# Optimization experiments

Measured on AMD Instinct MI355X. Metric: run time of the kernel, lower is better.

Reference implementation:

```python
import jax, jax.numpy as jnp
import numpy as np

B, U = 64, 512          # batch, max_units
CORE, UNIT = 512, 256   # core_output_size, unit_embedding_size
HID, ACT = 1024, 12     # hidden_layer_size, ACTION_COUNT


def setup_inputs() -> dict:
    key = jax.random.key(0)
    ks = jax.random.split(key, 6)
    core_output = jax.random.normal(ks[0], (B, 1, CORE), dtype=jnp.float32)
    own_unit_embeddings = jax.random.normal(ks[1], (B, U, UNIT), dtype=jnp.float32)
    nr_units = jax.random.randint(ks[2], (B, 1), 0, U, dtype=jnp.int32)
    nr_own_flags = jax.random.randint(ks[3], (B, 1), 0, 64, dtype=jnp.int32)
    W1 = jax.random.normal(ks[4], (CORE + UNIT, HID), dtype=jnp.float32) * (1.0 / np.sqrt(CORE + UNIT))
    b1 = jnp.zeros((HID,), dtype=jnp.float32)
    W2 = jax.random.normal(ks[5], (HID, ACT), dtype=jnp.float32) * (1.0 / np.sqrt(HID))
    b2 = jnp.zeros((ACT,), dtype=jnp.float32)
    return {"core_output": core_output, "own_unit_embeddings": own_unit_embeddings,
            "nr_units": nr_units, "nr_own_flags": nr_own_flags,
            "W1": W1, "b1": b1, "W2": W2, "b2": b2}


def reference(core_output, own_unit_embeddings, nr_units, nr_own_flags, W1, b1, W2, b2):
    b, u, _ = own_unit_embeddings.shape
    # broadcast core output to every unit slot and concat along features: [B, U, UNIT+CORE]
    core_rep = jnp.broadcast_to(core_output, (b, u, core_output.shape[-1]))
    combined = jnp.concatenate([own_unit_embeddings, core_rep], axis=-1)
    autoregressive_embedding = jax.nn.relu(jnp.einsum('buf,fh->buh', combined, W1) + b1)
    logits = jnp.einsum('buh,ha->bua', autoregressive_embedding, W2) + b2
    action_probs = jax.nn.softmax(logits, axis=-1)
    # vectorized range mask: mask[i, f:n, :] = 1 else 1e-9
    idx = jnp.arange(u, dtype=nr_units.dtype)[None, :]        # [1, U]
    valid = (idx >= nr_own_flags) & (idx < nr_units)          # [B, U]
    mask = jnp.where(valid, 1.0, 1e-9).astype(action_probs.dtype)[:, :, None]
    return action_probs * mask, autoregressive_embedding
```

## Files before the change

kernel.cpp:

```cpp
#include <hip/hip_runtime.h>
#include <hip/hip_fp16.h>
#include <cstdint>

typedef unsigned short ushort_t;
typedef _Float16 f16x8 __attribute__((ext_vector_type(8)));
typedef float f32x4 __attribute__((ext_vector_type(4)));
typedef unsigned int u32x4 __attribute__((ext_vector_type(4)));

#define M_TOT  32768
#define K_EMB  256
#define K_CORE 512
#define ACT    12

__device__ __forceinline__ unsigned int pack2h(float a, float b) {
    __half2 h = __floats2half2_rn(a, b);
    union { __half2 h2; unsigned int u; } v; v.h2 = h; return v.u;
}

__global__ __launch_bounds__(1024) void prep_k(const float* __restrict__ W1,
                                               ushort_t* __restrict__ W1T,
                                               const float* __restrict__ core,
                                               const float* __restrict__ b1,
                                               float* __restrict__ cp) {
    __shared__ float tile[64][65];
    __shared__ float part[3][256];
    const int id = blockIdx.x;
    const int t = threadIdx.x;
    if (id < 64) {
        const int k0 = (id & 3) * 64, n0 = (id >> 2) * 64;
        const int r = t >> 4, c4 = (t & 15) * 4;
        const float4 v = *(const float4*)(W1 + (size_t)(k0 + r) * 1024 + n0 + c4);
        tile[r][c4 + 0] = v.x; tile[r][c4 + 1] = v.y;
        tile[r][c4 + 2] = v.z; tile[r][c4 + 3] = v.w;
        __syncthreads();
        uint2 o;
        o.x = pack2h(tile[c4 + 0][r], tile[c4 + 1][r]);
        o.y = pack2h(tile[c4 + 2][r], tile[c4 + 3][r]);
        *(uint2*)(W1T + (size_t)(n0 + r) * 256 + k0 + c4) = o;
    } else {
        const int xb = id - 64;
        const int b = xb >> 2;
        const int nl = t & 255;
        const int n = (xb & 3) * 256 + nl;
        const int kq = t >> 8;
        const float* cr = core + (size_t)b * K_CORE + kq * 128;
        const float* wp = W1 + (size_t)(K_EMB + kq * 128) * 1024 + n;
        float s0 = 0.f, s1 = 0.f, s2 = 0.f, s3 = 0.f;
#pragma unroll 8
        for (int k = 0; k < 128; k += 4) {
            s0 += cr[k + 0] * wp[(size_t)(k + 0) * 1024];
            s1 += cr[k + 1] * wp[(size_t)(k + 1) * 1024];
            s2 += cr[k + 2] * wp[(size_t)(k + 2) * 1024];
            s3 += cr[k + 3] * wp[(size_t)(k + 3) * 1024];
        }
        const float s = (s0 + s1) + (s2 + s3);
        if (kq) part[kq - 1][nl] = s;
        __syncthreads();
        if (kq == 0)
            cp[b * 1024 + n] = b1[n] + s + part[0][nl] + part[1][nl] + part[2][nl];
    }
}

__global__ __launch_bounds__(256, 3) void fused_k(const float* __restrict__ emb,
                                                  const ushort_t* __restrict__ w1t,
                                                  const float* __restrict__ cp,
                                                  const float* __restrict__ W2,
                                                  const float* __restrict__ b2,
                                                  const int* __restrict__ nr_units,
                                                  const int* __restrict__ nr_flags,
                                                  float* __restrict__ out0,
                                                  float* __restrict__ out1) {
    __shared__ __align__(16) ushort_t Asl[64 * 256];
    __shared__ __align__(16) ushort_t Bsl[2][128 * 32];
    __shared__ __align__(16) float logitAcc[64][ACT];

    const int t = threadIdx.x;
    const int w = t >> 6, L = t & 63;
    const int lane16 = L & 15, qd = L >> 4;
    const int m0 = blockIdx.x * 64;
    const int bb = blockIdx.x >> 3;

    if (t < 192) ((f32x4*)logitAcc)[t] = (f32x4){0.f, 0.f, 0.f, 0.f};

    {
        const int g = t & 31;
        const int rsub = t >> 5;
#pragma unroll
        for (int p = 0; p < 8; ++p) {
            const int r = p * 8 + rsub;
            const float* src = emb + (size_t)(m0 + r) * K_EMB + g * 8;
            const f32x4 v0 = __builtin_nontemporal_load((const f32x4*)src);
            const f32x4 v1 = __builtin_nontemporal_load((const f32x4*)src + 1);
            u32x4 pk;
            pk[0] = pack2h(v0[0], v0[1]); pk[1] = pack2h(v0[2], v0[3]);
            pk[2] = pack2h(v1[0], v1[1]); pk[3] = pack2h(v1[2], v1[3]);
            *(u32x4*)((char*)Asl + r * 512 + ((g ^ (r & 7)) << 4)) = pk;
        }
    }

    const int rB = t >> 2, gB = t & 3;
    const ushort_t* gBa = w1t + (size_t)rB * K_EMB + gB * 8;
    const int wb0 = rB * 64 + ((gB ^ ((rB >> 1) & 3)) << 4);
    const int wb1 = wb0 + 64 * 64;

    {
        const u32x4 b0 = *(const u32x4*)gBa;
        const u32x4 b1v = *(const u32x4*)(gBa + 64 * K_EMB);
        *(u32x4*)((char*)Bsl + wb0) = b0;
        *(u32x4*)((char*)Bsl + wb1) = b1v;
    }
    __syncthreads();

    const int araw = lane16 * 512;
    const int axor = lane16 & 7;
    const int bswz = (qd ^ ((lane16 >> 1) & 3)) << 4;
    int boffc[2];
#pragma unroll
    for (int ni = 0; ni < 2; ++ni)
        boffc[ni] = (w * 32 + ni * 16 + lane16) * 64 + bswz;

    f32x4 acc[2][4];
#pragma unroll
    for (int ni = 0; ni < 2; ++ni)
#pragma unroll
        for (int mi = 0; mi < 4; ++mi) acc[ni][mi] = (f32x4){0.f, 0.f, 0.f, 0.f};
    f32x4 la[4][3];
#pragma unroll
    for (int mi = 0; mi < 4; ++mi)
#pragma unroll
        for (int c = 0; c < 3; ++c) la[mi][c] = (f32x4){0.f, 0.f, 0.f, 0.f};

    u32x4 pb0, pb1;
    int cur = 0;
    for (int it = 0; it < 64; ++it) {
        const int ks = it & 7;
        if (it < 63) {
            const int itn = it + 1;
            const size_t off = (size_t)(itn >> 3) * 128 * K_EMB + (size_t)(itn & 7) * 32;
            pb0 = *(const u32x4*)(gBa + off);
            pb1 = *(const u32x4*)(gBa + 64 * K_EMB + off);
        }
        const int ga = (((ks << 2) | qd) ^ axor) << 4;
        f16x8 af[4], bf[2];
#pragma unroll
        for (int mi = 0; mi < 4; ++mi)
            af[mi] = *(const f16x8*)((const char*)Asl + mi * 8192 + araw + ga);
        const char* bbase = (const char*)Bsl + cur * 8192;
#pragma unroll
        for (int ni = 0; ni < 2; ++ni)
            bf[ni] = *(const f16x8*)(bbase + boffc[ni]);
#pragma unroll
        for (int ni = 0; ni < 2; ++ni)
#pragma unroll
            for (int mi = 0; mi < 4; ++mi)
                acc[ni][mi] = __builtin_amdgcn_mfma_f32_16x16x32_f16(bf[ni], af[mi], acc[ni][mi], 0, 0, 0);

        if ((it & 7) == 7) {
            const int nt = it >> 3;
#pragma unroll
            for (int ni = 0; ni < 2; ++ni) {
                const int nbase = nt * 128 + w * 32 + ni * 16 + qd * 4;
                const f32x4 cpv = *(const f32x4*)(cp + bb * 1024 + nbase);
#pragma unroll
                for (int mi = 0; mi < 4; ++mi) {
                    f32x4 v = acc[ni][mi] + cpv;
#pragma unroll
                    for (int j = 0; j < 4; ++j) v[j] = v[j] > 0.f ? v[j] : 0.f;
                    acc[ni][mi] = v;
                    const size_t m = (size_t)(m0 + mi * 16 + lane16);
                    __builtin_nontemporal_store(v, (f32x4*)(out1 + m * 1024 + nbase));
                }
#pragma unroll
                for (int r = 0; r < 4; ++r) {
                    const f32x4* wp = (const f32x4*)(W2 + (size_t)(nbase + r) * ACT);
                    const f32x4 w2a = wp[0], w2b = wp[1], w2c = wp[2];
#pragma unroll
                    for (int mi = 0; mi < 4; ++mi) {
                        const float vv = acc[ni][mi][r];
                        la[mi][0] += w2a * vv;
                        la[mi][1] += w2b * vv;
                        la[mi][2] += w2c * vv;
                    }
                }
#pragma unroll
                for (int mi = 0; mi < 4; ++mi) acc[ni][mi] = (f32x4){0.f, 0.f, 0.f, 0.f};
            }
        }

        if (it < 63) {
            char* bnxt = (char*)Bsl + ((cur ^ 1) * 8192);
            *(u32x4*)(bnxt + wb0) = pb0;
            *(u32x4*)(bnxt + wb1) = pb1;
        }
        __syncthreads();
        cur ^= 1;
    }

#pragma unroll
    for (int mi = 0; mi < 4; ++mi)
#pragma unroll
        for (int c = 0; c < 3; ++c)
#pragma unroll
            for (int j = 0; j < 4; ++j) {
                la[mi][c][j] += __shfl_xor(la[mi][c][j], 16, 64);
                la[mi][c][j] += __shfl_xor(la[mi][c][j], 32, 64);
            }
    if (L < 16) {
#pragma unroll
        for (int mi = 0; mi < 4; ++mi) {
            const int row = mi * 16 + L;
#pragma unroll
            for (int c = 0; c < 3; ++c)
#pragma unroll
                for (int j = 0; j < 4; ++j)
                    atomicAdd(&logitAcc[row][c * 4 + j], la[mi][c][j]);
        }
    }
    __syncthreads();

    if (t < 64) {
        float lg[ACT];
#pragma unroll
        for (int a = 0; a < ACT; ++a) lg[a] = logitAcc[t][a] + b2[a];
        float mx = lg[0];
#pragma unroll
        for (int a = 1; a < ACT; ++a) mx = fmaxf(mx, lg[a]);
        float s = 0.f;
#pragma unroll
        for (int a = 0; a < ACT; ++a) { lg[a] = __expf(lg[a] - mx); s += lg[a]; }
        const float inv = 1.f / s;
        const int m = m0 + t;
        const int u = m & 511;
        const float msk = (u >= nr_flags[bb] && u < nr_units[bb]) ? 1.0f : 1e-9f;
        f32x4 o0, o1, o2;
#pragma unroll
        for (int j = 0; j < 4; ++j) {
            o0[j] = lg[j] * inv * msk;
            o1[j] = lg[j + 4] * inv * msk;
            o2[j] = lg[j + 8] * inv * msk;
        }
        f32x4* op = (f32x4*)(out0 + (size_t)m * ACT);
        __builtin_nontemporal_store(o0, op + 0);
        __builtin_nontemporal_store(o1, op + 1);
        __builtin_nontemporal_store(o2, op + 2);
    }
}

extern "C" void kernel_launch(void* const* d_in, const int* in_sizes, int n_in,
                              void* d_out, int out_size, void* d_ws, size_t ws_size,
                              hipStream_t stream) {
    const float* core   = (const float*)d_in[0];
    const float* emb    = (const float*)d_in[1];
    const int* nr_units = (const int*)d_in[2];
    const int* nr_flags = (const int*)d_in[3];
    const float* W1     = (const float*)d_in[4];
    const float* b1     = (const float*)d_in[5];
    const float* W2     = (const float*)d_in[6];
    const float* b2     = (const float*)d_in[7];

    float* out0 = (float*)d_out;
    float* out1 = out0 + (size_t)M_TOT * ACT;

    ushort_t* w1t = (ushort_t*)d_ws;
    float* cp = (float*)((char*)d_ws + (size_t)1024 * 256 * 2);

    prep_k<<<dim3(320), 1024, 0, stream>>>(W1, w1t, core, b1, cp);
    fused_k<<<dim3(512), 256, 0, stream>>>(emb, w1t, cp, W2, b2, nr_units, nr_flags, out0, out1);
}
```

Before: 256.9 us.

## Load W1 fragments directly from global memory instead of LDS double buffer

Removes the shared-memory double-buffered staging of the transposed W1 tile and the per-iteration block barrier. Each wave now reads its MFMA B fragments straight from global (L2-resident) memory, with the k-loop fully unrolled inside an n-tile loop. This cuts LDS traffic and the 64 __syncthreads per block, and frees LDS, which may raise occupancy. In exchange there is more global/L2 load traffic, since W1 is no longer shared across the four waves, and load latency is exposed with no explicit prefetch.

```diff
diff --git a/kernel.cpp b/kernel.cpp
--- a/kernel.cpp
+++ b/kernel.cpp
@@ -71,7 +71,6 @@
                                                   float* __restrict__ out0,
                                                   float* __restrict__ out1) {
     __shared__ __align__(16) ushort_t Asl[64 * 256];
-    __shared__ __align__(16) ushort_t Bsl[2][128 * 32];
     __shared__ __align__(16) float logitAcc[64][ACT];
 
     const int t = threadIdx.x;
@@ -97,103 +96,69 @@
             *(u32x4*)((char*)Asl + r * 512 + ((g ^ (r & 7)) << 4)) = pk;
         }
     }
-
-    const int rB = t >> 2, gB = t & 3;
-    const ushort_t* gBa = w1t + (size_t)rB * K_EMB + gB * 8;
-    const int wb0 = rB * 64 + ((gB ^ ((rB >> 1) & 3)) << 4);
-    const int wb1 = wb0 + 64 * 64;
-
-    {
-        const u32x4 b0 = *(const u32x4*)gBa;
-        const u32x4 b1v = *(const u32x4*)(gBa + 64 * K_EMB);
-        *(u32x4*)((char*)Bsl + wb0) = b0;
-        *(u32x4*)((char*)Bsl + wb1) = b1v;
-    }
     __syncthreads();
 
     const int araw = lane16 * 512;
     const int axor = lane16 & 7;
-    const int bswz = (qd ^ ((lane16 >> 1) & 3)) << 4;
-    int boffc[2];
-#pragma unroll
-    for (int ni = 0; ni < 2; ++ni)
-        boffc[ni] = (w * 32 + ni * 16 + lane16) * 64 + bswz;
-
-    f32x4 acc[2][4];
-#pragma unroll
-    for (int ni = 0; ni < 2; ++ni)
-#pragma unroll
-        for (int mi = 0; mi < 4; ++mi) acc[ni][mi] = (f32x4){0.f, 0.f, 0.f, 0.f};
+    const ushort_t* gB = w1t + (size_t)(w * 32 + lane16) * 256 + qd * 8;
+
     f32x4 la[4][3];
 #pragma unroll
     for (int mi = 0; mi < 4; ++mi)
 #pragma unroll
         for (int c = 0; c < 3; ++c) la[mi][c] = (f32x4){0.f, 0.f, 0.f, 0.f};
 
-    u32x4 pb0, pb1;
-    int cur = 0;
-    for (int it = 0; it < 64; ++it) {
-        const int ks = it & 7;
-        if (it < 63) {
-            const int itn = it + 1;
-            const size_t off = (size_t)(itn >> 3) * 128 * K_EMB + (size_t)(itn & 7) * 32;
-            pb0 = *(const u32x4*)(gBa + off);
-            pb1 = *(const u32x4*)(gBa + 64 * K_EMB + off);
-        }
-        const int ga = (((ks << 2) | qd) ^ axor) << 4;
-        f16x8 af[4], bf[2];
-#pragma unroll
-        for (int mi = 0; mi < 4; ++mi)
-            af[mi] = *(const f16x8*)((const char*)Asl + mi * 8192 + araw + ga);
-        const char* bbase = (const char*)Bsl + cur * 8192;
+    for (int nt = 0; nt < 8; ++nt) {
+        f32x4 acc[2][4];
 #pragma unroll
         for (int ni = 0; ni < 2; ++ni)
-            bf[ni] = *(const f16x8*)(bbase + boffc[ni]);
-#pragma unroll
-        for (int ni = 0; ni < 2; ++ni)
+#pragma unroll
+            for (int mi = 0; mi < 4; ++mi) acc[ni][mi] = (f32x4){0.f, 0.f, 0.f, 0.f};
+
+        const ushort_t* gBt = gB + (size_t)nt * 128 * 256;
+#pragma unroll
+        for (int ks = 0; ks < 8; ++ks) {
+            const f16x8 bf0 = *(const f16x8*)(gBt + ks * 32);
+            const f16x8 bf1 = *(const f16x8*)(gBt + ks * 32 + 16 * 256);
+            const int ga = (((ks << 2) | qd) ^ axor) << 4;
+            f16x8 af[4];
 #pragma unroll
             for (int mi = 0; mi < 4; ++mi)
-                acc[ni][mi] = __builtin_amdgcn_mfma_f32_16x16x32_f16(bf[ni], af[mi], acc[ni][mi], 0, 0, 0);
-
-        if ((it & 7) == 7) {
-            const int nt = it >> 3;
-#pragma unroll
-            for (int ni = 0; ni < 2; ++ni) {
-                const int nbase = nt * 128 + w * 32 + ni * 16 + qd * 4;
-                const f32x4 cpv = *(const f32x4*)(cp + bb * 1024 + nbase);
+                af[mi] = *(const f16x8*)((const char*)Asl + mi * 8192 + araw + ga);
+#pragma unroll
+            for (int mi = 0; mi < 4; ++mi)
+                acc[0][mi] = __builtin_amdgcn_mfma_f32_16x16x32_f16(bf0, af[mi], acc[0][mi], 0, 0, 0);
+#pragma unroll
+            for (int mi = 0; mi < 4; ++mi)
+                acc[1][mi] = __builtin_amdgcn_mfma_f32_16x16x32_f16(bf1, af[mi], acc[1][mi], 0, 0, 0);
+        }
+
+#pragma unroll
+        for (int ni = 0; ni < 2; ++ni) {
+            const int nbase = nt * 128 + w * 32 + ni * 16 + qd * 4;
+            const f32x4 cpv = *(const f32x4*)(cp + bb * 1024 + nbase);
+#pragma unroll
+            for (int mi = 0; mi < 4; ++mi) {
+                f32x4 v = acc[ni][mi] + cpv;
+#pragma unroll
+                for (int j = 0; j < 4; ++j) v[j] = v[j] > 0.f ? v[j] : 0.f;
+                acc[ni][mi] = v;
+                const size_t m = (size_t)(m0 + mi * 16 + lane16);
+                __builtin_nontemporal_store(v, (f32x4*)(out1 + m * 1024 + nbase));
+            }
+#pragma unroll
+            for (int r = 0; r < 4; ++r) {
+                const f32x4* wp = (const f32x4*)(W2 + (size_t)(nbase + r) * ACT);
+                const f32x4 w2a = wp[0], w2b = wp[1], w2c = wp[2];
 #pragma unroll
                 for (int mi = 0; mi < 4; ++mi) {
-                    f32x4 v = acc[ni][mi] + cpv;
-#pragma unroll
-                    for (int j = 0; j < 4; ++j) v[j] = v[j] > 0.f ? v[j] : 0.f;
-                    acc[ni][mi] = v;
-                    const size_t m = (size_t)(m0 + mi * 16 + lane16);
-                    __builtin_nontemporal_store(v, (f32x4*)(out1 + m * 1024 + nbase));
+                    const float vv = acc[ni][mi][r];
+                    la[mi][0] += w2a * vv;
+                    la[mi][1] += w2b * vv;
+                    la[mi][2] += w2c * vv;
                 }
-#pragma unroll
-                for (int r = 0; r < 4; ++r) {
-                    const f32x4* wp = (const f32x4*)(W2 + (size_t)(nbase + r) * ACT);
-                    const f32x4 w2a = wp[0], w2b = wp[1], w2c = wp[2];
-#pragma unroll
-                    for (int mi = 0; mi < 4; ++mi) {
-                        const float vv = acc[ni][mi][r];
-                        la[mi][0] += w2a * vv;
-                        la[mi][1] += w2b * vv;
-                        la[mi][2] += w2c * vv;
-                    }
-                }
-#pragma unroll
-                for (int mi = 0; mi < 4; ++mi) acc[ni][mi] = (f32x4){0.f, 0.f, 0.f, 0.f};
             }
         }
-
-        if (it < 63) {
-            char* bnxt = (char*)Bsl + ((cur ^ 1) * 8192);
-            *(u32x4*)(bnxt + wb0) = pb0;
-            *(u32x4*)(bnxt + wb1) = pb1;
-        }
-        __syncthreads();
-        cur ^= 1;
     }
 
 #pragma unroll
```

New measurement: 303.6 us. 18.2% more time.
